# Kernel optimization log

Hardware: AMD Instinct MI355X
Metric: run time of the kernel (lower is better)

## Reference

```python
import jax, jax.numpy as jnp
import numpy as np

NUM_ITER = 3
NUM_SLOTS = 8
SLOT_SIZE = 128
MLP_HIDDEN = 256
EPSILON = 1e-8
INPUT_SIZE = 128
LN_EPS = 1e-5


def layer_norm(x):
    # parameter-free LayerNorm over last dim (LayerNorm() built with no args)
    mu = jnp.mean(x, axis=-1, keepdims=True)
    var = jnp.mean(jnp.square(x - mu), axis=-1, keepdims=True)
    return (x - mu) * jax.lax.rsqrt(var + LN_EPS)


def setup_inputs() -> dict:
    key = jax.random.key(0)
    ks = jax.random.split(key, 16)
    B, N, Din, D, H = 128, 4096, INPUT_SIZE, SLOT_SIZE, MLP_HIDDEN
    s_in = 1.0 / np.sqrt(Din)
    s_d = 1.0 / np.sqrt(D)
    s_h = 1.0 / np.sqrt(H)
    return {
        "inputs": jax.random.normal(ks[0], (B, N, Din), jnp.float32),
        "slots_noise": jax.random.normal(ks[1], (B, NUM_SLOTS, D), jnp.float32),
        "slots_mu": jax.random.normal(ks[2], (1, 1, D), jnp.float32),
        "slots_log_sigma": jax.random.normal(ks[3], (1, 1, D), jnp.float32) * 0.1,
        "Wq": jax.random.normal(ks[4], (D, D), jnp.float32) * s_d,
        "Wk": jax.random.normal(ks[5], (D, Din), jnp.float32) * s_in,
        "Wv": jax.random.normal(ks[6], (D, Din), jnp.float32) * s_in,
        "W_ih": jax.random.normal(ks[7], (3 * D, D), jnp.float32) * s_d,
        "W_hh": jax.random.normal(ks[8], (3 * D, D), jnp.float32) * s_d,
        "b_ih": jax.random.normal(ks[9], (3 * D,), jnp.float32) * s_d,
        "b_hh": jax.random.normal(ks[10], (3 * D,), jnp.float32) * s_d,
        "W1": jax.random.normal(ks[11], (H, D), jnp.float32) * s_d,
        "b1": jnp.zeros((H,), jnp.float32),
        "W2": jax.random.normal(ks[12], (D, H), jnp.float32) * s_h,
        "b2": jnp.zeros((D,), jnp.float32),
    }


def gru_cell(x, h, W_ih, W_hh, b_ih, b_hh):
    # PyTorch GRU, single step. x, h: (..., D)
    gx = x @ W_ih.T + b_ih  # (..., 3D)
    gh = h @ W_hh.T + b_hh
    D = h.shape[-1]
    xr, xz, xn = gx[..., :D], gx[..., D:2 * D], gx[..., 2 * D:]
    hr, hz, hn = gh[..., :D], gh[..., D:2 * D], gh[..., 2 * D:]
    r = jax.nn.sigmoid(xr + hr)
    z = jax.nn.sigmoid(xz + hz)
    n = jnp.tanh(xn + r * hn)
    return (1.0 - z) * n + z * h


def reference(inputs, slots_noise, slots_mu, slots_log_sigma, Wq, Wk, Wv,
              W_ih, W_hh, b_ih, b_hh, W1, b1, W2, b2):
    scale = 1.0 / np.sqrt(SLOT_SIZE)
    x = layer_norm(inputs)                      # (B, N, Din)
    k = x @ Wk.T                                # (B, N, D)
    v = x @ Wv.T                                # (B, N, D)
    slots = slots_mu + jnp.exp(slots_log_sigma) * slots_noise  # (B, S, D)
    for _ in range(NUM_ITER):
        slots_n = layer_norm(slots)             # NOTE: GRU hidden is the NORMED slots (matches source)
        q = slots_n @ Wq.T                      # (B, S, D)
        logits = jnp.einsum("bnd,bsd->bns", k, q) * scale  # (B, N, S)
        attn = jax.nn.softmax(logits, axis=-1) + EPSILON
        attn = attn / jnp.sum(attn, axis=-2, keepdims=True)
        updates = jnp.einsum("bns,bnd->bsd", attn, v)      # (B, S, D)
        slots = gru_cell(updates, slots_n, W_ih, W_hh, b_ih, b_hh)
        slots = slots + (jax.nn.relu(layer_norm(slots) @ W1.T + b1) @ W2.T + b2)
    return slots
```

## Files before the change

kernel.cpp:

```cpp
#include <hip/hip_runtime.h>
#include <math.h>


typedef __attribute__((ext_vector_type(4))) float fx4;
typedef __attribute__((ext_vector_type(8))) short sx8;
typedef __attribute__((ext_vector_type(4))) short sx4;
typedef __attribute__((ext_vector_type(8))) __bf16 bfx8;
typedef __attribute__((ext_vector_type(4))) unsigned short ux4;

static __device__ __forceinline__ fx4 MFMA(sx8 a, sx8 b, fx4 c) {
  return __builtin_amdgcn_mfma_f32_16x16x32_bf16(
      __builtin_bit_cast(bfx8, a), __builtin_bit_cast(bfx8, b), c, 0, 0, 0);
}

static __device__ __forceinline__ unsigned short f2bf(float f) {
  union { float f; unsigned u; } x; x.f = f;
  unsigned r = x.u + 0x7fffu + ((x.u >> 16) & 1u);
  return (unsigned short)(r >> 16);
}
static __device__ __forceinline__ float bf2f(unsigned short u) {
  union { unsigned u; float f; } x; x.u = ((unsigned)u) << 16; return x.f;
}
static __device__ __forceinline__ fx4 ntload4(const float* p) {
  return __builtin_nontemporal_load((const fx4*)p);
}

#define PSTR 72

__global__ __launch_bounds__(256) void k_fold(
    const float* __restrict__ Wq, const float* __restrict__ Wk,
    const float* __restrict__ Wih, const float* __restrict__ Wv,
    float* __restrict__ Wqk, float* __restrict__ Wihv) {
  int idx = blockIdx.x * 256 + threadIdx.x;
  if (idx < 16384) {
    int e = idx >> 7, c = idx & 127;
    float s = 0.f;
#pragma unroll 4
    for (int d = 0; d < 128; d++) s += Wq[d * 128 + e] * Wk[d * 128 + c];
    Wqk[idx] = s * 0.08838834764831845f;
    return;
  }
  idx -= 16384;
// ... 1 lines not shown
    int g = idx >> 7, c = idx & 127;
    float s = 0.f;
#pragma unroll 4
    for (int d = 0; d < 128; d++) s += Wih[g * 128 + d] * Wv[d * 128 + c];
    Wihv[idx] = s;
  }
}

__global__ __launch_bounds__(256) void k_pack(
    const float* __restrict__ noise, const float* __restrict__ mu,
    const float* __restrict__ lsig, const float* __restrict__ Wqk,
    const float* __restrict__ Wihv, const float* __restrict__ Whh,
    const float* __restrict__ W1, const float* __restrict__ W2,
    float* __restrict__ slots, unsigned short* __restrict__ wqk_b,
    unsigned short* __restrict__ wihv_b, unsigned short* __restrict__ whh_b,
    unsigned short* __restrict__ w1_b, unsigned short* __restrict__ w2_b) {
  int idx = blockIdx.x * 256 + threadIdx.x;
  if (idx < 131072) {
    int d = idx & 127;
    slots[idx] = mu[d] + expf(lsig[d]) * noise[idx];
    return;
  }
  idx -= 131072;
  if (idx < 16384) {
    wqk_b[idx] = f2bf(Wqk[(idx & 127) * 128 + (idx >> 7)]);
    return;
  }
  idx -= 16384;
  if (idx < 49152) { wihv_b[idx] = f2bf(Wihv[idx]); return; }
  idx -= 49152;
  if (idx < 49152) { whh_b[idx] = f2bf(Whh[idx]); return; }
  idx -= 49152;
  if (idx < 32768) { w1_b[idx] = f2bf(W1[idx]); return; }
  idx -= 32768;
  w2_b[idx] = f2bf(W2[idx]);
}

__global__ __launch_bounds__(64) void k_slot_pre(
    const float* __restrict__ slots, const unsigned short* __restrict__ wqk_b,
    float* __restrict__ slots_n, unsigned short* __restrict__ q2_b) {
  __shared__ __align__(16) short xf[4 * 64 * 8];
  int l = threadIdx.x;
  int r = l & 15, seg = l >> 4;
  long rowbase = (long)blockIdx.x * 16;
  {
    const float* xp = slots + (rowbase + r) * 128 + seg * 32;
    float* snp = slots_n + (rowbase + r) * 128 + seg * 32;
    float v[32];
    float s = 0.f, s2 = 0.f;
#pragma unroll
// ... 33 lines not shown
    sx8 a = *(const sx8*)&xf[(ks * 64 + l) * 8];
#pragma unroll
    for (int nt = 0; nt < 8; nt++) {
      sx8 bfr = *(const sx8*)(wqk_b + (nt * 16 + (l & 15)) * 128 + ks * 32 + (l >> 4) * 8);
      acc[nt] = MFMA(a, bfr, acc[nt]);
    }
  }
  int cl = l & 15, rq = (l >> 4) * 4;
#pragma unroll
  for (int nt = 0; nt < 8; nt++)
#pragma unroll
    for (int rg = 0; rg < 4; rg++)
      q2_b[(rowbase + rq + rg) * 128 + nt * 16 + cl] = f2bf(acc[nt][rg]);
}

__global__ __launch_bounds__(256, 4) void k_attn(
    const unsigned short* __restrict__ ln16, const unsigned short* __restrict__ q2b,
    float* __restrict__ upd_part, float* __restrict__ sattn_part) {
  __shared__ __align__(16) float abuf[4 * 1024];
  __shared__ __align__(16) short plds[4][2][16 * PSTR];
  __shared__ float sattnbuf[4 * 8];
  int tid = threadIdx.x, w = tid >> 6, l = tid & 63;
  int b = blockIdx.x >> 4, c = blockIdx.x & 15;
  long base = (long)b * 4096 + (c * 4 + w) * 64;
  const unsigned short* xt = ln16 + base * 128;
  int nr = l & 15, seg = l >> 4, qd = seg * 8;
  sx8 qf[4];
#pragma unroll
  for (int ks = 0; ks < 4; ks++) {
    if (nr < 8) {
      qf[ks] = *(const sx8*)(q2b + ((long)b * 8 + nr) * 128 + ks * 32 + qd);
    } else {
      sx8 t;
#pragma unroll
      for (int j = 0; j < 8; j++) t[j] = 0;
      qf[ks] = t;
    }
  }
  const fx4 z4 = {0.f, 0.f, 0.f, 0.f};
  float satacc[4] = {0.f, 0.f, 0.f, 0.f};
  short* ph = &plds[w][0][0];
  short* pl = &plds[w][1][0];
#pragma unroll
  for (int mt = 0; mt < 4; mt++) {
    fx4 cc = z4;
#pragma unroll
    for (int ks = 0; ks < 4; ks++) {
      sx8 bfr = *(const sx8*)(xt + (mt * 16 + nr) * 128 + ks * 32 + qd);
      cc = MFMA(qf[ks], bfr, cc);
    }
    float m01 = fmaxf(fmaxf(cc[0], cc[1]), fmaxf(cc[2], cc[3]));
    m01 = fmaxf(m01, __shfl_xor(m01, 16, 64));
    float p0 = __expf(cc[0] - m01), p1 = __expf(cc[1] - m01),
          p2 = __expf(cc[2] - m01), p3 = __expf(cc[3] - m01);
    float sl = p0 + p1 + p2 + p3;
    sl += __shfl_xor(sl, 16, 64);
    float inv = 1.f / sl;
    float at0 = p0 * inv + 1e-8f, at1 = p1 * inv + 1e-8f;
    float at2 = p2 * inv + 1e-8f, at3 = p3 * inv + 1e-8f;
    satacc[0] += at0; satacc[1] += at1; satacc[2] += at2; satacc[3] += at3;
    int pbase = mt * 16 + nr;
    unsigned short h0 = f2bf(at0), h1 = f2bf(at1), h2 = f2bf(at2), h3 = f2bf(at3);
    ph[(seg * 4 + 0) * PSTR + pbase] = (short)h0;
    ph[(seg * 4 + 1) * PSTR + pbase] = (short)h1;
    ph[(seg * 4 + 2) * PSTR + pbase] = (short)h2;
    ph[(seg * 4 + 3) * PSTR + pbase] = (short)h3;
    pl[(seg * 4 + 0) * PSTR + pbase] = (short)f2bf(at0 - bf2f(h0));
    pl[(seg * 4 + 1) * PSTR + pbase] = (short)f2bf(at1 - bf2f(h1));
    pl[(seg * 4 + 2) * PSTR + pbase] = (short)f2bf(at2 - bf2f(h2));
    pl[(seg * 4 + 3) * PSTR + pbase] = (short)f2bf(at3 - bf2f(h3));
  }
  fx4 acc[8];
#pragma unroll
  for (int nt = 0; nt < 8; nt++) acc[nt] = z4;
#pragma unroll
  for (int ks2 = 0; ks2 < 2; ks2++) {
    sx8 pah = *(const sx8*)&ph[nr * PSTR + ks2 * 32 + seg * 8];
    sx8 pal = *(const sx8*)&pl[nr * PSTR + ks2 * 32 + seg * 8];
#pragma unroll
    for (int nt = 0; nt < 8; nt++) {
      const unsigned short* cp = xt + (ks2 * 32 + seg * 8) * 128 + nt * 16 + nr;
      sx8 bfr;
#pragma unroll
      for (int j = 0; j < 8; j++) bfr[j] = (short)cp[j * 128];
      acc[nt] = MFMA(pah, bfr, acc[nt]);
// ... 14 lines not shown
    v += __shfl_xor(v, 2, 64);
    v += __shfl_xor(v, 4, 64);
    v += __shfl_xor(v, 8, 64);
    if (nr == 0 && seg < 2) sattnbuf[w * 8 + seg * 4 + rg] = v;
  }
  __syncthreads();
  {
    int i = tid * 4;
    fx4 o = *(const fx4*)&abuf[i] + *(const fx4*)&abuf[1024 + i] +
            *(const fx4*)&abuf[2048 + i] + *(const fx4*)&abuf[3072 + i];
    *(fx4*)(upd_part + ((size_t)(b * 16 + c)) * 1024 + i) = o;
    if (tid < 8)
      sattn_part[(b * 16 + c) * 8 + tid] =
          sattnbuf[tid] + sattnbuf[8 + tid] + sattnbuf[16 + tid] + sattnbuf[24 + tid];
  }
}

__global__ __launch_bounds__(256, 4) void k_attn_first(
    const float* __restrict__ x, unsigned short* __restrict__ ln16,
    const unsigned short* __restrict__ q2b,
    float* __restrict__ upd_part, float* __restrict__ sattn_part) {
  __shared__ __align__(16) float abuf[4 * 1024];
  __shared__ __align__(16) short plds[4][2][16 * PSTR];
  __shared__ float sattnbuf[4 * 8];
  int tid = threadIdx.x, w = tid >> 6, l = tid & 63;
  int b = blockIdx.x >> 4, c = blockIdx.x & 15;
  long base = (long)b * 4096 + (c * 4 + w) * 64;
  const float* xs = x + base * 128;
  unsigned short* xt = ln16 + base * 128;
  int nr = l & 15, seg = l >> 4, qd = seg * 8;
  sx8 qf[4];
#pragma unroll
  for (int ks = 0; ks < 4; ks++) {
    if (nr < 8) {
      qf[ks] = *(const sx8*)(q2b + ((long)b * 8 + nr) * 128 + ks * 32 + qd);
    } else {
      sx8 t;
#pragma unroll
      for (int j = 0; j < 8; j++) t[j] = 0;
      qf[ks] = t;
    }
  }
  const fx4 z4 = {0.f, 0.f, 0.f, 0.f};
  float satacc[4] = {0.f, 0.f, 0.f, 0.f};
  short* ph = &plds[w][0][0];
  short* pl = &plds[w][1][0];
#pragma unroll
  for (int mt = 0; mt < 4; mt++) {
    const float* rp = xs + (mt * 16 + nr) * 128 + qd;
    float v[32];
    float sm = 0.f, s2 = 0.f;
#pragma unroll
    for (int ks = 0; ks < 4; ks++) {
      fx4 t0 = ntload4(rp + ks * 32);
      fx4 t1 = ntload4(rp + ks * 32 + 4);
      v[ks * 8 + 0] = t0.x; v[ks * 8 + 1] = t0.y; v[ks * 8 + 2] = t0.z; v[ks * 8 + 3] = t0.w;
      v[ks * 8 + 4] = t1.x; v[ks * 8 + 5] = t1.y; v[ks * 8 + 6] = t1.z; v[ks * 8 + 7] = t1.w;
      sm += t0.x + t0.y + t0.z + t0.w + t1.x + t1.y + t1.z + t1.w;
      s2 += t0.x * t0.x + t0.y * t0.y + t0.z * t0.z + t0.w * t0.w +
            t1.x * t1.x + t1.y * t1.y + t1.z * t1.z + t1.w * t1.w;
    }
// ... 8 lines not shown
#pragma unroll
      for (int j = 0; j < 8; j++) t[j] = (short)f2bf((v[ks * 8 + j] - mean) * rstd);
      *(sx8*)(xt + (mt * 16 + nr) * 128 + ks * 32 + qd) = t;
      cc = MFMA(qf[ks], t, cc);
    }
    float m01 = fmaxf(fmaxf(cc[0], cc[1]), fmaxf(cc[2], cc[3]));
    m01 = fmaxf(m01, __shfl_xor(m01, 16, 64));
    float p0 = __expf(cc[0] - m01), p1 = __expf(cc[1] - m01),
          p2 = __expf(cc[2] - m01), p3 = __expf(cc[3] - m01);
    float sl = p0 + p1 + p2 + p3;
    sl += __shfl_xor(sl, 16, 64);
    float inv = 1.f / sl;
    float at0 = p0 * inv + 1e-8f, at1 = p1 * inv + 1e-8f;
    float at2 = p2 * inv + 1e-8f, at3 = p3 * inv + 1e-8f;
    satacc[0] += at0; satacc[1] += at1; satacc[2] += at2; satacc[3] += at3;
    int pbase = mt * 16 + nr;
    unsigned short h0 = f2bf(at0), h1 = f2bf(at1), h2 = f2bf(at2), h3 = f2bf(at3);
    ph[(seg * 4 + 0) * PSTR + pbase] = (short)h0;
    ph[(seg * 4 + 1) * PSTR + pbase] = (short)h1;
    ph[(seg * 4 + 2) * PSTR + pbase] = (short)h2;
    ph[(seg * 4 + 3) * PSTR + pbase] = (short)h3;
    pl[(seg * 4 + 0) * PSTR + pbase] = (short)f2bf(at0 - bf2f(h0));
    pl[(seg * 4 + 1) * PSTR + pbase] = (short)f2bf(at1 - bf2f(h1));
    pl[(seg * 4 + 2) * PSTR + pbase] = (short)f2bf(at2 - bf2f(h2));
    pl[(seg * 4 + 3) * PSTR + pbase] = (short)f2bf(at3 - bf2f(h3));
  }
  __threadfence_block();
  fx4 acc[8];
#pragma unroll
  for (int nt = 0; nt < 8; nt++) acc[nt] = z4;
#pragma unroll
  for (int ks2 = 0; ks2 < 2; ks2++) {
    sx8 pah = *(const sx8*)&ph[nr * PSTR + ks2 * 32 + seg * 8];
    sx8 pal = *(const sx8*)&pl[nr * PSTR + ks2 * 32 + seg * 8];
#pragma unroll
    for (int nt = 0; nt < 8; nt++) {
      const unsigned short* cp = xt + (ks2 * 32 + seg * 8) * 128 + nt * 16 + nr;
      sx8 bfr;
#pragma unroll
      for (int j = 0; j < 8; j++) bfr[j] = (short)cp[j * 128];
// ... 15 lines not shown
    v += __shfl_xor(v, 2, 64);
    v += __shfl_xor(v, 4, 64);
    v += __shfl_xor(v, 8, 64);
    if (nr == 0 && seg < 2) sattnbuf[w * 8 + seg * 4 + rg] = v;
  }
  __syncthreads();
  {
    int i = tid * 4;
    fx4 o = *(const fx4*)&abuf[i] + *(const fx4*)&abuf[1024 + i] +
            *(const fx4*)&abuf[2048 + i] + *(const fx4*)&abuf[3072 + i];
    *(fx4*)(upd_part + ((size_t)(b * 16 + c)) * 1024 + i) = o;
    if (tid < 8)
      sattn_part[(b * 16 + c) * 8 + tid] =
          sattnbuf[tid] + sattnbuf[8 + tid] + sattnbuf[16 + tid] + sattnbuf[24 + tid];
  }
}

__global__ __launch_bounds__(256) void k_slot_post(
    const float* __restrict__ upd_part, const float* __restrict__ sattn_part,
    float* __restrict__ slots_n,
    const unsigned short* __restrict__ wihv_b, const unsigned short* __restrict__ whh_b,
    const float* __restrict__ b_ih, const float* __restrict__ b_hh,
    const unsigned short* __restrict__ w1_b, const float* __restrict__ b1,
    const unsigned short* __restrict__ w2_b, const float* __restrict__ b2,
    const unsigned short* __restrict__ wqk_b,
    unsigned short* __restrict__ q2_b, float* __restrict__ out_final, int final_flag) {
  __shared__ __align__(16) char smem[78336];
  float* gx = (float*)smem;
  float* gh = (float*)(smem + 24576);
  float* xred = gx;
  short* xfr = (short*)(smem + 49152);
  short* hfr = (short*)(smem + 53248);
  short* ynf = (short*)(smem + 57344);
  short* y1f = (short*)(smem + 61440);
  float* snew = (float*)(smem + 69632);
  float* satred = (float*)(smem + 78080);
  int tid = threadIdx.x, w = tid >> 6, l = tid & 63;
  int rowbase = blockIdx.x * 16;
  int r = l & 15, seg = l >> 4;
  {
    int row = rowbase + r;
    int bb = row >> 3, ss = row & 7;
    float a[32];
#pragma unroll
    for (int i = 0; i < 32; i++) a[i] = 0.f;
    float satsum = 0.f;
#pragma unroll
    for (int ci = 0; ci < 4; ci++) {
      int ch = bb * 16 + w * 4 + ci;
      const float* up = upd_part + (size_t)ch * 1024 + ss * 128 + seg * 32;
#pragma unroll
      for (int i = 0; i < 8; i++) {
        fx4 t = *(const fx4*)(up + i * 4);
        a[i * 4 + 0] += t.x; a[i * 4 + 1] += t.y; a[i * 4 + 2] += t.z; a[i * 4 + 3] += t.w;
      }
      satsum += sattn_part[ch * 8 + ss];
    }
#pragma unroll
    for (int i = 0; i < 8; i++) {
      fx4 t = {a[i * 4], a[i * 4 + 1], a[i * 4 + 2], a[i * 4 + 3]};
      *(fx4*)&xred[w * 2048 + r * 128 + seg * 32 + i * 4] = t;
    }
    if (seg == 0) satred[w * 16 + r] = satsum;
  }
  __syncthreads();
  if (w == 0) {
    float inv = 1.f / (satred[r] + satred[16 + r] + satred[32 + r] + satred[48 + r]);
    float a[32];
#pragma unroll
    for (int i = 0; i < 8; i++) {
      fx4 t = *(const fx4*)&xred[r * 128 + seg * 32 + i * 4];
      fx4 t1 = *(const fx4*)&xred[2048 + r * 128 + seg * 32 + i * 4];
      fx4 t2 = *(const fx4*)&xred[4096 + r * 128 + seg * 32 + i * 4];
      fx4 t3 = *(const fx4*)&xred[6144 + r * 128 + seg * 32 + i * 4];
      t = t + t1 + t2 + t3;
      a[i * 4 + 0] = t.x * inv; a[i * 4 + 1] = t.y * inv;
      a[i * 4 + 2] = t.z * inv; a[i * 4 + 3] = t.w * inv;
    }
#pragma unroll
    for (int q = 0; q < 4; q++) {
      sx8 t;
#pragma unroll
      for (int j = 0; j < 8; j++) t[j] = (short)f2bf(a[q * 8 + j]);
      *(sx8*)&xfr[(seg * 64 + (r + 16 * q)) * 8] = t;
    }
  } else if (w == 1) {
    const float* hp = slots_n + (long)(rowbase + r) * 128 + seg * 32;
#pragma unroll
    for (int q = 0; q < 4; q++) {
      fx4 t0 = *(const fx4*)(hp + q * 8);
      fx4 t1 = *(const fx4*)(hp + q * 8 + 4);
      sx8 t;
      t[0] = (short)f2bf(t0.x); t[1] = (short)f2bf(t0.y);
      t[2] = (short)f2bf(t0.z); t[3] = (short)f2bf(t0.w);
      t[4] = (short)f2bf(t1.x); t[5] = (short)f2bf(t1.y);
      t[6] = (short)f2bf(t1.z); t[7] = (short)f2bf(t1.w);
      *(sx8*)&hfr[(seg * 64 + (r + 16 * q)) * 8] = t;
    }
  }
  __syncthreads();
  const fx4 z4 = {0.f, 0.f, 0.f, 0.f};
  {
    fx4 ax[6], ah[6];
#pragma unroll
    for (int j = 0; j < 6; j++) { ax[j] = z4; ah[j] = z4; }
#pragma unroll
    for (int ks = 0; ks < 4; ks++) {
      sx8 a_x = *(const sx8*)&xfr[(ks * 64 + l) * 8];
      sx8 a_h = *(const sx8*)&hfr[(ks * 64 + l) * 8];
#pragma unroll
      for (int j = 0; j < 6; j++) {
        int nt = w * 6 + j;
        sx8 bx = *(const sx8*)(wihv_b + (nt * 16 + (l & 15)) * 128 + ks * 32 + (l >> 4) * 8);
        sx8 bh = *(const sx8*)(whh_b + (nt * 16 + (l & 15)) * 128 + ks * 32 + (l >> 4) * 8);
        ax[j] = MFMA(a_x, bx, ax[j]);
        ah[j] = MFMA(a_h, bh, ah[j]);
      }
    }
#pragma unroll
    for (int j = 0; j < 6; j++) {
      int col = (w * 6 + j) * 16 + (l & 15);
#pragma unroll
      for (int rg = 0; rg < 4; rg++) {
        int row = (l >> 4) * 4 + rg;
        gx[row * 384 + col] = ax[j][rg];
        gh[row * 384 + col] = ah[j][rg];
      }
    }
  }
  __syncthreads();
  {
    int row = tid >> 4, j0 = (tid & 15) * 8;
#pragma unroll
    for (int j = j0; j < j0 + 8; j++) {
      float xr = gx[row * 384 + j] + b_ih[j];
      float xz = gx[row * 384 + 128 + j] + b_ih[128 + j];
      float xn = gx[row * 384 + 256 + j] + b_ih[256 + j];
      float hr = gh[row * 384 + j] + b_hh[j];
      float hz = gh[row * 384 + 128 + j] + b_hh[128 + j];
      float hn = gh[row * 384 + 256 + j] + b_hh[256 + j];
      float rr = 1.f / (1.f + __expf(-(xr + hr)));
      float zz = 1.f / (1.f + __expf(-(xz + hz)));
      float nn = tanhf(xn + rr * hn);
      float h = slots_n[(long)(rowbase + row) * 128 + j];
      snew[row * 132 + j] = (1.f - zz) * nn + zz * h;
    }
  }
  __syncthreads();
  if (w == 0) {
    float v[32];
    float s = 0.f, s2 = 0.f;
#pragma unroll
    for (int i = 0; i < 32; i++) {
      float t = snew[r * 132 + seg * 32 + i];
      v[i] = t; s += t; s2 += t * t;
    }
    s += __shfl_xor(s, 16, 64);  s += __shfl_xor(s, 32, 64);
    s2 += __shfl_xor(s2, 16, 64); s2 += __shfl_xor(s2, 32, 64);
    float mean = s * 0.0078125f;
    float var = s2 * 0.0078125f - mean * mean;
    float rstd = rsqrtf(var + 1e-5f);
#pragma unroll
    for (int q = 0; q < 4; q++) {
      sx8 t;
#pragma unroll
      for (int j = 0; j < 8; j++) t[j] = (short)f2bf((v[q * 8 + j] - mean) * rstd);
      *(sx8*)&ynf[(seg * 64 + (r + 16 * q)) * 8] = t;
    }
  }
  __syncthreads();
  {
    fx4 y[4];
#pragma unroll
    for (int j = 0; j < 4; j++) y[j] = z4;
#pragma unroll
    for (int ks = 0; ks < 4; ks++) {
      sx8 a = *(const sx8*)&ynf[(ks * 64 + l) * 8];
#pragma unroll
      for (int j = 0; j < 4; j++) {
        int nt = w * 4 + j;
        sx8 bf = *(const sx8*)(w1_b + (nt * 16 + (l & 15)) * 128 + ks * 32 + (l >> 4) * 8);
        y[j] = MFMA(a, bf, y[j]);
      }
    }
#pragma unroll
    for (int j = 0; j < 4; j++) {
      int col = (w * 4 + j) * 16 + (l & 15);
      float bias = b1[col];
      int ks3 = col >> 5, qq = (col >> 3) & 3, jj = col & 7;
#pragma unroll
      for (int rg = 0; rg < 4; rg++) {
        float val = fmaxf(y[j][rg] + bias, 0.f);
        int m = (l >> 4) * 4 + rg;
        y1f[(ks3 * 64 + m + 16 * qq) * 8 + jj] = (short)f2bf(val);
      }
    }
  }
  __syncthreads();
  {
    fx4 zz2[2];
    zz2[0] = z4; zz2[1] = z4;
#pragma unroll
    for (int ks = 0; ks < 8; ks++) {
      sx8 a = *(const sx8*)&y1f[(ks * 64 + l) * 8];
#pragma unroll
      for (int j = 0; j < 2; j++) {
        sx8 bf = *(const sx8*)(w2_b + ((w * 2 + j) * 16 + (l & 15)) * 256 + ks * 32 + (l >> 4) * 8);
        zz2[j] = MFMA(a, bf, zz2[j]);
      }
    }
#pragma unroll
    for (int j = 0; j < 2; j++) {
      int col = (w * 2 + j) * 16 + (l & 15);
      float bias = b2[col];
#pragma unroll
      for (int rg = 0; rg < 4; rg++) {
        int row = (l >> 4) * 4 + rg;
        snew[row * 132 + col] += zz2[j][rg] + bias;
      }
    }
  }
  __syncthreads();
  if (final_flag) {
    int row = tid >> 4, c8 = (tid & 15) * 8;
    fx4 t0 = *(const fx4*)&snew[row * 132 + c8];
    fx4 t1 = *(const fx4*)&snew[row * 132 + c8 + 4];
    *(fx4*)(out_final + (long)(rowbase + row) * 128 + c8) = t0;
    *(fx4*)(out_final + (long)(rowbase + row) * 128 + c8 + 4) = t1;
    return;
  }
  if (w == 0) {
    float v[32];
    float s = 0.f, s2 = 0.f;
#pragma unroll
    for (int i = 0; i < 32; i++) {
      float t = snew[r * 132 + seg * 32 + i];
      v[i] = t; s += t; s2 += t * t;
    }
    s += __shfl_xor(s, 16, 64);  s += __shfl_xor(s, 32, 64);
    s2 += __shfl_xor(s2, 16, 64); s2 += __shfl_xor(s2, 32, 64);
    float mean = s * 0.0078125f;
    float var = s2 * 0.0078125f - mean * mean;
    float rstd = rsqrtf(var + 1e-5f);
    float* snp = slots_n + (long)(rowbase + r) * 128 + seg * 32;
#pragma unroll
    for (int i = 0; i < 8; i++) {
      fx4 t = {(v[i * 4 + 0] - mean) * rstd, (v[i * 4 + 1] - mean) * rstd,
               (v[i * 4 + 2] - mean) * rstd, (v[i * 4 + 3] - mean) * rstd};
      *(fx4*)(snp + i * 4) = t;
      v[i * 4 + 0] = t.x; v[i * 4 + 1] = t.y; v[i * 4 + 2] = t.z; v[i * 4 + 3] = t.w;
    }
#pragma unroll
    for (int q = 0; q < 4; q++) {
      sx8 t;
#pragma unroll
      for (int j = 0; j < 8; j++) t[j] = (short)f2bf(v[q * 8 + j]);
      *(sx8*)&ynf[(seg * 64 + (r + 16 * q)) * 8] = t;
    }
  }
  __syncthreads();
  {
    fx4 acc2[2];
    acc2[0] = z4; acc2[1] = z4;
#pragma unroll
    for (int ks = 0; ks < 4; ks++) {
      sx8 a = *(const sx8*)&ynf[(ks * 64 + l) * 8];
#pragma unroll
      for (int j = 0; j < 2; j++) {
        int nt = w * 2 + j;
        sx8 bf = *(const sx8*)(wqk_b + (nt * 16 + (l & 15)) * 128 + ks * 32 + (l >> 4) * 8);
        acc2[j] = MFMA(a, bf, acc2[j]);
      }
    }
    int cl = l & 15, rq = (l >> 4) * 4;
#pragma unroll
    for (int j = 0; j < 2; j++) {
      int nt = w * 2 + j;
#pragma unroll
      for (int rg = 0; rg < 4; rg++)
        q2_b[(long)(rowbase + rq + rg) * 128 + nt * 16 + cl] = f2bf(acc2[j][rg]);
    }
  }
}

extern "C" void kernel_launch(void* const* d_in, const int* in_sizes, int n_in,
                              void* d_out, int out_size, void* d_ws, size_t ws_size,
                              hipStream_t stream) {
  (void)in_sizes; (void)n_in; (void)out_size; (void)ws_size;
  const float* x = (const float*)d_in[0];
  const float* noise = (const float*)d_in[1];
  const float* mu = (const float*)d_in[2];
  const float* lsig = (const float*)d_in[3];
  const float* Wq = (const float*)d_in[4];
  const float* Wk = (const float*)d_in[5];
  const float* Wv = (const float*)d_in[6];
  const float* Wih = (const float*)d_in[7];
  const float* Whh = (const float*)d_in[8];
// ... 12 lines not shown
    return p;
  };
  unsigned short* ln16 = (unsigned short*)take(134217728);
  float* Wqk = (float*)take(65536);
  float* Wihv = (float*)take(196608);
  unsigned short* wqk_b = (unsigned short*)take(32768);
  unsigned short* wihv_b = (unsigned short*)take(98304);
  unsigned short* whh_b = (unsigned short*)take(98304);
  unsigned short* w1_b = (unsigned short*)take(65536);
  unsigned short* w2_b = (unsigned short*)take(65536);
  float* slots = (float*)take(524288);
  float* slots_n = (float*)take(524288);
  unsigned short* q2_b = (unsigned short*)take(262144);
  float* upd_part = (float*)take(8388608);
  float* sattn_part = (float*)take(65536);

  k_fold<<<256, 256, 0, stream>>>(Wq, Wk, Wih, Wv, Wqk, Wihv);
  k_pack<<<1216, 256, 0, stream>>>(noise, mu, lsig, Wqk, Wihv, Whh, W1, W2,
                                   slots, wqk_b, wihv_b, whh_b, w1_b, w2_b);
  k_slot_pre<<<64, 64, 0, stream>>>(slots, wqk_b, slots_n, q2_b);
  k_attn_first<<<2048, 256, 0, stream>>>(x, ln16, q2_b, upd_part, sattn_part);
  k_slot_post<<<64, 256, 0, stream>>>(upd_part, sattn_part, slots_n, wihv_b, whh_b,
                                      b_ih, b_hh, w1_b, b1, w2_b, b2, wqk_b,
                                      q2_b, (float*)d_out, 0);
  for (int it = 1; it < 3; it++) {
    k_attn<<<2048, 256, 0, stream>>>(ln16, q2_b, upd_part, sattn_part);
    k_slot_post<<<64, 256, 0, stream>>>(upd_part, sattn_part, slots_n, wihv_b, whh_b,
                                        b_ih, b_hh, w1_b, b1, w2_b, b2, wqk_b,
                                        q2_b, (float*)d_out, (it == 2) ? 1 : 0);
  }
}
```

Measured before the change: 577.8 us.

## Fuse slot update into attention kernel via last-block atomic counter

Removes the separate k_slot_post launches by having the last finishing attention block of each group of two batches (32 blocks, 16 slot rows) run the GRU, MLP and next-query computation, signalled by an atomic counter that k_pack zeroes. It also reworks the GRU so each wave computes its r/z/n gate tiles in registers and applies the gates directly, dropping the large shared-memory staging of gx and gh. This cuts launch gaps and the tail of the small 64-block slot kernel, allowing slot updates to overlap with other attention blocks. The trade-offs are threadfence plus atomic overhead in every block, and the slot work running inside the attention kernel's shared-memory and occupancy limits.

```diff
diff --git a/kernel.cpp b/kernel.cpp
--- a/kernel.cpp
+++ b/kernel.cpp
@@ -26,6 +26,7 @@
 }
 
 #define PSTR 72
+#define SMEM_BYTES 34944
 
 __global__ __launch_bounds__(256) void k_fold(
     const float* __restrict__ Wq, const float* __restrict__ Wk,
@@ -57,7 +58,8 @@
     const float* __restrict__ W1, const float* __restrict__ W2,
     float* __restrict__ slots, unsigned short* __restrict__ wqk_b,
     unsigned short* __restrict__ wihv_b, unsigned short* __restrict__ whh_b,
-    unsigned short* __restrict__ w1_b, unsigned short* __restrict__ w2_b) {
+    unsigned short* __restrict__ w1_b, unsigned short* __restrict__ w2_b,
+    unsigned* __restrict__ cnt) {
   int idx = blockIdx.x * 256 + threadIdx.x;
   if (idx < 131072) {
     int d = idx & 127;
@@ -76,7 +78,9 @@
   idx -= 49152;
   if (idx < 32768) { w1_b[idx] = f2bf(W1[idx]); return; }
   idx -= 32768;
-  w2_b[idx] = f2bf(W2[idx]);
+  if (idx < 32768) { w2_b[idx] = f2bf(W2[idx]); return; }
+  idx -= 32768;
+  if (idx < 192) cnt[idx] = 0;
 }
 
 __global__ __launch_bounds__(64) void k_slot_pre(
@@ -140,12 +144,253 @@
       q2_b[(rowbase + rq + rg) * 128 + nt * 16 + cl] = f2bf(acc[nt][rg]);
 }
 
-__global__ __launch_bounds__(256, 4) void k_attn(
+static __device__ __forceinline__ void slot_post_body(
+    char* smem, int tid, int rowbase,
+    const float* __restrict__ upd_part, const float* __restrict__ sattn_part,
+    float* __restrict__ slots_n,
+    const unsigned short* __restrict__ wihv_b, const unsigned short* __restrict__ whh_b,
+    const float* __restrict__ b_ih, const float* __restrict__ b_hh,
+    const unsigned short* __restrict__ w1_b, const float* __restrict__ b1,
+    const unsigned short* __restrict__ w2_b, const float* __restrict__ b2,
+    const unsigned short* __restrict__ wqk_b, unsigned short* __restrict__ q2_b,
+    float* __restrict__ out_final, int final_flag) {
+  short* xfr = (short*)smem;
+  short* hfr = (short*)(smem + 4096);
+  short* ynf = (short*)(smem + 8192);
+  short* y1f = (short*)(smem + 12288);
+  float* snew = (float*)(smem + 20480);
+  float* satred = (float*)(smem + 28928);
+  int w = tid >> 6, l = tid & 63;
+  int r = l & 15, seg = l >> 4;
+  const fx4 z4 = {0.f, 0.f, 0.f, 0.f};
+  {
+    int tr = tid & 15, tc = tid >> 4;
+    int row = rowbase + tr;
+    int bb = row >> 3, ss = row & 7;
+    fx4 a0 = z4, a1 = z4;
+#pragma unroll 4
+    for (int ci = 0; ci < 16; ci++) {
+      const float* up = upd_part + (size_t)(bb * 16 + ci) * 1024 + ss * 128 + tc * 8;
+      a0 += *(const fx4*)up;
+      a1 += *(const fx4*)(up + 4);
+    }
+    if (tc == 0) {
+      float ssum = 0.f;
+#pragma unroll 4
+      for (int ci = 0; ci < 16; ci++) ssum += sattn_part[(bb * 16 + ci) * 8 + ss];
+      satred[tr] = ssum;
+    }
+    {
+      const float* hp = slots_n + (long)row * 128 + tc * 8;
+      fx4 t0 = *(const fx4*)hp, t1 = *(const fx4*)(hp + 4);
+      sx8 t;
+      t[0] = (short)f2bf(t0.x); t[1] = (short)f2bf(t0.y);
+      t[2] = (short)f2bf(t0.z); t[3] = (short)f2bf(t0.w);
+      t[4] = (short)f2bf(t1.x); t[5] = (short)f2bf(t1.y);
+      t[6] = (short)f2bf(t1.z); t[7] = (short)f2bf(t1.w);
+      int ks = tc >> 2, q = tc & 3;
+      *(sx8*)&hfr[(ks * 64 + tr + 16 * q) * 8] = t;
+    }
+    __syncthreads();
+    float inv = 1.f / satred[tr];
+    sx8 t;
+    t[0] = (short)f2bf(a0.x * inv); t[1] = (short)f2bf(a0.y * inv);
+    t[2] = (short)f2bf(a0.z * inv); t[3] = (short)f2bf(a0.w * inv);
+    t[4] = (short)f2bf(a1.x * inv); t[5] = (short)f2bf(a1.y * inv);
+    t[6] = (short)f2bf(a1.z * inv); t[7] = (short)f2bf(a1.w * inv);
+    int ks = tc >> 2, q = tc & 3;
+    *(sx8*)&xfr[(ks * 64 + tr + 16 * q) * 8] = t;
+  }
+  __syncthreads();
+  {
+    fx4 ax[6], ah[6];
+#pragma unroll
+    for (int j = 0; j < 6; j++) { ax[j] = z4; ah[j] = z4; }
+    int cl = l & 15;
+#pragma unroll
+    for (int ks = 0; ks < 4; ks++) {
+      sx8 a_x = *(const sx8*)&xfr[(ks * 64 + l) * 8];
+      sx8 a_h = *(const sx8*)&hfr[(ks * 64 + l) * 8];
+#pragma unroll
+      for (int j = 0; j < 6; j++) {
+        int nt = w * 2 + (j & 1) + (j >> 1) * 8;
+        sx8 bx = *(const sx8*)(wihv_b + (nt * 16 + cl) * 128 + ks * 32 + seg * 8);
+        sx8 bh = *(const sx8*)(whh_b + (nt * 16 + cl) * 128 + ks * 32 + seg * 8);
+        ax[j] = MFMA(a_x, bx, ax[j]);
+        ah[j] = MFMA(a_h, bh, ah[j]);
+      }
+    }
+#pragma unroll
+    for (int jj = 0; jj < 2; jj++) {
+      int col = (w * 2 + jj) * 16 + cl;
+      float bir = b_ih[col], biz = b_ih[128 + col], bin = b_ih[256 + col];
+      float bhr = b_hh[col], bhz = b_hh[128 + col], bhn = b_hh[256 + col];
+#pragma unroll
+      for (int rg = 0; rg < 4; rg++) {
+        int row = seg * 4 + rg;
+        float xr = ax[jj][rg] + bir, xz = ax[jj + 2][rg] + biz, xnn = ax[jj + 4][rg] + bin;
+        float hr = ah[jj][rg] + bhr, hz = ah[jj + 2][rg] + bhz, hnn = ah[jj + 4][rg] + bhn;
+        float rr = 1.f / (1.f + __expf(-(xr + hr)));
+        float zz = 1.f / (1.f + __expf(-(xz + hz)));
+        float nn = tanhf(xnn + rr * hnn);
+        float h = slots_n[(long)(rowbase + row) * 128 + col];
+        snew[row * 132 + col] = (1.f - zz) * nn + zz * h;
+      }
+    }
+  }
+  __syncthreads();
+  if (w == 0) {
+    float v[32];
+    float s = 0.f, s2 = 0.f;
+#pragma unroll
+    for (int i = 0; i < 32; i++) {
+      float t = snew[r * 132 + seg * 32 + i];
+      v[i] = t; s += t; s2 += t * t;
+    }
+    s += __shfl_xor(s, 16, 64);  s += __shfl_xor(s, 32, 64);
+    s2 += __shfl_xor(s2, 16, 64); s2 += __shfl_xor(s2, 32, 64);
+    float mean = s * 0.0078125f;
+    float var = s2 * 0.0078125f - mean * mean;
+    float rstd = rsqrtf(var + 1e-5f);
+#pragma unroll
+    for (int q = 0; q < 4; q++) {
+      sx8 t;
+#pragma unroll
+      for (int j = 0; j < 8; j++) t[j] = (short)f2bf((v[q * 8 + j] - mean) * rstd);
+      *(sx8*)&ynf[(seg * 64 + (r + 16 * q)) * 8] = t;
+    }
+  }
+  __syncthreads();
+  {
+    fx4 y[4];
+#pragma unroll
+    for (int j = 0; j < 4; j++) y[j] = z4;
+#pragma unroll
+    for (int ks = 0; ks < 4; ks++) {
+      sx8 a = *(const sx8*)&ynf[(ks * 64 + l) * 8];
+#pragma unroll
+      for (int j = 0; j < 4; j++) {
+        int nt = w * 4 + j;
+        sx8 bf = *(const sx8*)(w1_b + (nt * 16 + (l & 15)) * 128 + ks * 32 + (l >> 4) * 8);
+        y[j] = MFMA(a, bf, y[j]);
+      }
+    }
+#pragma unroll
+    for (int j = 0; j < 4; j++) {
+      int col = (w * 4 + j) * 16 + (l & 15);
+      float bias = b1[col];
+      int ks3 = col >> 5, qq = (col >> 3) & 3, jj = col & 7;
+#pragma unroll
+      for (int rg = 0; rg < 4; rg++) {
+        float val = fmaxf(y[j][rg] + bias, 0.f);
+        int m = (l >> 4) * 4 + rg;
+        y1f[(ks3 * 64 + m + 16 * qq) * 8 + jj] = (short)f2bf(val);
+      }
+    }
+  }
+  __syncthreads();
+  {
+    fx4 zz2[2];
+    zz2[0] = z4; zz2[1] = z4;
+#pragma unroll
+    for (int ks = 0; ks < 8; ks++) {
+      sx8 a = *(const sx8*)&y1f[(ks * 64 + l) * 8];
+#pragma unroll
+      for (int j = 0; j < 2; j++) {
+        sx8 bf = *(const sx8*)(w2_b + ((w * 2 + j) * 16 + (l & 15)) * 256 + ks * 32 + (l >> 4) * 8);
+        zz2[j] = MFMA(a, bf, zz2[j]);
+      }
+    }
+#pragma unroll
+    for (int j = 0; j < 2; j++) {
+      int col = (w * 2 + j) * 16 + (l & 15);
+      float bias = b2[col];
+#pragma unroll
+      for (int rg = 0; rg < 4; rg++) {
+        int row = (l >> 4) * 4 + rg;
+        snew[row * 132 + col] += zz2[j][rg] + bias;
+      }
+    }
+  }
+  __syncthreads();
+  if (final_flag) {
+    int row = tid >> 4, c8 = (tid & 15) * 8;
+    fx4 t0 = *(const fx4*)&snew[row * 132 + c8];
+    fx4 t1 = *(const fx4*)&snew[row * 132 + c8 + 4];
+    *(fx4*)(out_final + (long)(rowbase + row) * 128 + c8) = t0;
+    *(fx4*)(out_final + (long)(rowbase + row) * 128 + c8 + 4) = t1;
+    return;
+  }
+  if (w == 0) {
+    float v[32];
+    float s = 0.f, s2 = 0.f;
+#pragma unroll
+    for (int i = 0; i < 32; i++) {
+      float t = snew[r * 132 + seg * 32 + i];
+      v[i] = t; s += t; s2 += t * t;
+    }
+    s += __shfl_xor(s, 16, 64);  s += __shfl_xor(s, 32, 64);
+    s2 += __shfl_xor(s2, 16, 64); s2 += __shfl_xor(s2, 32, 64);
+    float mean = s * 0.0078125f;
+    float var = s2 * 0.0078125f - mean * mean;
+    float rstd = rsqrtf(var + 1e-5f);
+    float* snp = slots_n + (long)(rowbase + r) * 128 + seg * 32;
+#pragma unroll
+    for (int i = 0; i < 8; i++) {
+      fx4 t = {(v[i * 4 + 0] - mean) * rstd, (v[i * 4 + 1] - mean) * rstd,
+               (v[i * 4 + 2] - mean) * rstd, (v[i * 4 + 3] - mean) * rstd};
+      *(fx4*)(snp + i * 4) = t;
+      v[i * 4 + 0] = t.x; v[i * 4 + 1] = t.y; v[i * 4 + 2] = t.z; v[i * 4 + 3] = t.w;
+    }
+#pragma unroll
+    for (int q = 0; q < 4; q++) {
+      sx8 t;
+#pragma unroll
+      for (int j = 0; j < 8; j++) t[j] = (short)f2bf(v[q * 8 + j]);
+      *(sx8*)&ynf[(seg * 64 + (r + 16 * q)) * 8] = t;
+    }
+  }
+  __syncthreads();
+  {
+    fx4 acc2[2];
+    acc2[0] = z4; acc2[1] = z4;
+#pragma unroll
+    for (int ks = 0; ks < 4; ks++) {
+      sx8 a = *(const sx8*)&ynf[(ks * 64 + l) * 8];
+#pragma unroll
+      for (int j = 0; j < 2; j++) {
+        int nt = w * 2 + j;
+        sx8 bf = *(const sx8*)(wqk_b + (nt * 16 + (l & 15)) * 128 + ks * 32 + (l >> 4) * 8);
+        acc2[j] = MFMA(a, bf, acc2[j]);
+      }
+    }
+    int cl = l & 15, rq = (l >> 4) * 4;
+#pragma unroll
+    for (int j = 0; j < 2; j++) {
+      int nt = w * 2 + j;
+#pragma unroll
+      for (int rg = 0; rg < 4; rg++)
+        q2_b[(long)(rowbase + rq + rg) * 128 + nt * 16 + cl] = f2bf(acc2[j][rg]);
+    }
+  }
+}
+
+__global__ __launch_bounds__(256, 4) void k_iter(
     const unsigned short* __restrict__ ln16, const unsigned short* __restrict__ q2b,
-    float* __restrict__ upd_part, float* __restrict__ sattn_part) {
-  __shared__ __align__(16) float abuf[4 * 1024];
-  __shared__ __align__(16) short plds[4][2][16 * PSTR];
-  __shared__ float sattnbuf[4 * 8];
+    float* __restrict__ upd_part, float* __restrict__ sattn_part,
+    unsigned* __restrict__ pcnt,
+    float* __restrict__ slots_n,
+    const unsigned short* __restrict__ wihv_b, const unsigned short* __restrict__ whh_b,
+    const float* __restrict__ b_ih, const float* __restrict__ b_hh,
+    const unsigned short* __restrict__ w1_b, const float* __restrict__ b1,
+    const unsigned short* __restrict__ w2_b, const float* __restrict__ b2,
+    const unsigned short* __restrict__ wqk_b, unsigned short* __restrict__ q2_b,
+    float* __restrict__ out_final, int final_flag) {
+  __shared__ __align__(16) char smem[SMEM_BYTES];
+  __shared__ unsigned tail_done;
+  float* abuf = (float*)smem;
+  short* pbase = (short*)(smem + 16384);
+  float* sattnbuf = (float*)(smem + 16384 + 18432);
   int tid = threadIdx.x, w = tid >> 6, l = tid & 63;
   int b = blockIdx.x >> 4, c = blockIdx.x & 15;
   long base = (long)b * 4096 + (c * 4 + w) * 64;
@@ -165,8 +410,8 @@
   }
   const fx4 z4 = {0.f, 0.f, 0.f, 0.f};
   float satacc[4] = {0.f, 0.f, 0.f, 0.f};
-  short* ph = &plds[w][0][0];
-  short* pl = &plds[w][1][0];
+  short* ph = pbase + (w * 2) * (16 * PSTR);
+  short* pl = pbase + (w * 2 + 1) * (16 * PSTR);
 #pragma unroll
   for (int mt = 0; mt < 4; mt++) {
     fx4 cc = z4;
@@ -185,16 +430,16 @@
     float at0 = p0 * inv + 1e-8f, at1 = p1 * inv + 1e-8f;
     float at2 = p2 * inv + 1e-8f, at3 = p3 * inv + 1e-8f;
     satacc[0] += at0; satacc[1] += at1; satacc[2] += at2; satacc[3] += at3;
-    int pbase = mt * 16 + nr;
+    int pb = mt * 16 + nr;
     unsigned short h0 = f2bf(at0), h1 = f2bf(at1), h2 = f2bf(at2), h3 = f2bf(at3);
-    ph[(seg * 4 + 0) * PSTR + pbase] = (short)h0;
-    ph[(seg * 4 + 1) * PSTR + pbase] = (short)h1;
-    ph[(seg * 4 + 2) * PSTR + pbase] = (short)h2;
-    ph[(seg * 4 + 3) * PSTR + pbase] = (short)h3;
-    pl[(seg * 4 + 0) * PSTR + pbase] = (short)f2bf(at0 - bf2f(h0));
-    pl[(seg * 4 + 1) * PSTR + pbase] = (short)f2bf(at1 - bf2f(h1));
-    pl[(seg * 4 + 2) * PSTR + pbase] = (short)f2bf(at2 - bf2f(h2));
-    pl[(seg * 4 + 3) * PSTR + pbase] = (short)f2bf(at3 - bf2f(h3));
+    ph[(seg * 4 + 0) * PSTR + pb] = (short)h0;
+    ph[(seg * 4 + 1) * PSTR + pb] = (short)h1;
+    ph[(seg * 4 + 2) * PSTR + pb] = (short)h2;
+    ph[(seg * 4 + 3) * PSTR + pb] = (short)h3;
+    pl[(seg * 4 + 0) * PSTR + pb] = (short)f2bf(at0 - bf2f(h0));
+    pl[(seg * 4 + 1) * PSTR + pb] = (short)f2bf(at1 - bf2f(h1));
+    pl[(seg * 4 + 2) * PSTR + pb] = (short)f2bf(at2 - bf2f(h2));
+    pl[(seg * 4 + 3) * PSTR + pb] = (short)f2bf(at3 - bf2f(h3));
   }
   fx4 acc[8];
 #pragma unroll
@@ -239,15 +484,33 @@
       sattn_part[(b * 16 + c) * 8 + tid] =
           sattnbuf[tid] + sattnbuf[8 + tid] + sattnbuf[16 + tid] + sattnbuf[24 + tid];
   }
-}
-
-__global__ __launch_bounds__(256, 4) void k_attn_first(
+  __threadfence();
+  if (tid == 0) tail_done = (atomicAdd(&pcnt[b >> 1], 1u) == 31u) ? 1u : 0u;
+  __syncthreads();
+  if (!tail_done) return;
+  __threadfence();
+  slot_post_body(smem, tid, (b >> 1) * 16, upd_part, sattn_part, slots_n,
+                 wihv_b, whh_b, b_ih, b_hh, w1_b, b1, w2_b, b2, wqk_b, q2_b,
+                 out_final, final_flag);
+}
+
+__global__ __launch_bounds__(256, 4) void k_iter_first(
     const float* __restrict__ x, unsigned short* __restrict__ ln16,
     const unsigned short* __restrict__ q2b,
-    float* __restrict__ upd_part, float* __restrict__ sattn_part) {
-  __shared__ __align__(16) float abuf[4 * 1024];
-  __shared__ __align__(16) short plds[4][2][16 * PSTR];
-  __shared__ float sattnbuf[4 * 8];
+    float* __restrict__ upd_part, float* __restrict__ sattn_part,
+    unsigned* __restrict__ pcnt,
+    float* __restrict__ slots_n,
+    const unsigned short* __restrict__ wihv_b, const unsigned short* __restrict__ whh_b,
+    const float* __restrict__ b_ih, const float* __restrict__ b_hh,
+    const unsigned short* __restrict__ w1_b, const float* __restrict__ b1,
+    const unsigned short* __restrict__ w2_b, const float* __restrict__ b2,
+    const unsigned short* __restrict__ wqk_b, unsigned short* __restrict__ q2_b,
+    float* __restrict__ out_final, int final_flag) {
+  __shared__ __align__(16) char smem[SMEM_BYTES];
+  __shared__ unsigned tail_done;
+  float* abuf = (float*)smem;
+  short* pbase = (short*)(smem + 16384);
+  float* sattnbuf = (float*)(smem + 16384 + 18432);
   int tid = threadIdx.x, w = tid >> 6, l = tid & 63;
   int b = blockIdx.x >> 4, c = blockIdx.x & 15;
   long base = (long)b * 4096 + (c * 4 + w) * 64;
@@ -268,8 +531,8 @@
   }
   const fx4 z4 = {0.f, 0.f, 0.f, 0.f};
   float satacc[4] = {0.f, 0.f, 0.f, 0.f};
-  short* ph = &plds[w][0][0];
-  short* pl = &plds[w][1][0];
+  short* ph = pbase + (w * 2) * (16 * PSTR);
+  short* pl = pbase + (w * 2 + 1) * (16 * PSTR);
 #pragma unroll
   for (int mt = 0; mt < 4; mt++) {
     const float* rp = xs + (mt * 16 + nr) * 128 + qd;
@@ -308,16 +571,16 @@
     float at0 = p0 * inv + 1e-8f, at1 = p1 * inv + 1e-8f;
     float at2 = p2 * inv + 1e-8f, at3 = p3 * inv + 1e-8f;
     satacc[0] += at0; satacc[1] += at1; satacc[2] += at2; satacc[3] += at3;
-    int pbase = mt * 16 + nr;
+    int pb = mt * 16 + nr;
     unsigned short h0 = f2bf(at0), h1 = f2bf(at1), h2 = f2bf(at2), h3 = f2bf(at3);
-    ph[(seg * 4 + 0) * PSTR + pbase] = (short)h0;
-    ph[(seg * 4 + 1) * PSTR + pbase] = (short)h1;
-    ph[(seg * 4 + 2) * PSTR + pbase] = (short)h2;
-    ph[(seg * 4 + 3) * PSTR + pbase] = (short)h3;
-    pl[(seg * 4 + 0) * PSTR + pbase] = (short)f2bf(at0 - bf2f(h0));
-    pl[(seg * 4 + 1) * PSTR + pbase] = (short)f2bf(at1 - bf2f(h1));
-    pl[(seg * 4 + 2) * PSTR + pbase] = (short)f2bf(at2 - bf2f(h2));
-    pl[(seg * 4 + 3) * PSTR + pbase] = (short)f2bf(at3 - bf2f(h3));
+    ph[(seg * 4 + 0) * PSTR + pb] = (short)h0;
+    ph[(seg * 4 + 1) * PSTR + pb] = (short)h1;
+    ph[(seg * 4 + 2) * PSTR + pb] = (short)h2;
+    ph[(seg * 4 + 3) * PSTR + pb] = (short)h3;
+    pl[(seg * 4 + 0) * PSTR + pb] = (short)f2bf(at0 - bf2f(h0));
+    pl[(seg * 4 + 1) * PSTR + pb] = (short)f2bf(at1 - bf2f(h1));
+    pl[(seg * 4 + 2) * PSTR + pb] = (short)f2bf(at2 - bf2f(h2));
+    pl[(seg * 4 + 3) * PSTR + pb] = (short)f2bf(at3 - bf2f(h3));
   }
   __threadfence_block();
   fx4 acc[8];
@@ -363,273 +626,14 @@
       sattn_part[(b * 16 + c) * 8 + tid] =
           sattnbuf[tid] + sattnbuf[8 + tid] + sattnbuf[16 + tid] + sattnbuf[24 + tid];
   }
-}
-
-__global__ __launch_bounds__(256) void k_slot_post(
-    const float* __restrict__ upd_part, const float* __restrict__ sattn_part,
-    float* __restrict__ slots_n,
-    const unsigned short* __restrict__ wihv_b, const unsigned short* __restrict__ whh_b,
-    const float* __restrict__ b_ih, const float* __restrict__ b_hh,
-    const unsigned short* __restrict__ w1_b, const float* __restrict__ b1,
-    const unsigned short* __restrict__ w2_b, const float* __restrict__ b2,
-    const unsigned short* __restrict__ wqk_b,
-    unsigned short* __restrict__ q2_b, float* __restrict__ out_final, int final_flag) {
-  __shared__ __align__(16) char smem[78336];
-  float* gx = (float*)smem;
-  float* gh = (float*)(smem + 24576);
-  float* xred = gx;
-  short* xfr = (short*)(smem + 49152);
-  short* hfr = (short*)(smem + 53248);
-  short* ynf = (short*)(smem + 57344);
-  short* y1f = (short*)(smem + 61440);
-  float* snew = (float*)(smem + 69632);
-  float* satred = (float*)(smem + 78080);
-  int tid = threadIdx.x, w = tid >> 6, l = tid & 63;
-  int rowbase = blockIdx.x * 16;
-  int r = l & 15, seg = l >> 4;
-  {
-    int row = rowbase + r;
-    int bb = row >> 3, ss = row & 7;
-    float a[32];
-#pragma unroll
-    for (int i = 0; i < 32; i++) a[i] = 0.f;
-    float satsum = 0.f;
-#pragma unroll
-    for (int ci = 0; ci < 4; ci++) {
-      int ch = bb * 16 + w * 4 + ci;
-      const float* up = upd_part + (size_t)ch * 1024 + ss * 128 + seg * 32;
-#pragma unroll
-      for (int i = 0; i < 8; i++) {
-        fx4 t = *(const fx4*)(up + i * 4);
-        a[i * 4 + 0] += t.x; a[i * 4 + 1] += t.y; a[i * 4 + 2] += t.z; a[i * 4 + 3] += t.w;
-      }
-      satsum += sattn_part[ch * 8 + ss];
-    }
-#pragma unroll
-    for (int i = 0; i < 8; i++) {
-      fx4 t = {a[i * 4], a[i * 4 + 1], a[i * 4 + 2], a[i * 4 + 3]};
-      *(fx4*)&xred[w * 2048 + r * 128 + seg * 32 + i * 4] = t;
-    }
-    if (seg == 0) satred[w * 16 + r] = satsum;
-  }
-  __syncthreads();
-  if (w == 0) {
-    float inv = 1.f / (satred[r] + satred[16 + r] + satred[32 + r] + satred[48 + r]);
-    float a[32];
-#pragma unroll
-    for (int i = 0; i < 8; i++) {
-      fx4 t = *(const fx4*)&xred[r * 128 + seg * 32 + i * 4];
-      fx4 t1 = *(const fx4*)&xred[2048 + r * 128 + seg * 32 + i * 4];
-      fx4 t2 = *(const fx4*)&xred[4096 + r * 128 + seg * 32 + i * 4];
-      fx4 t3 = *(const fx4*)&xred[6144 + r * 128 + seg * 32 + i * 4];
-      t = t + t1 + t2 + t3;
-      a[i * 4 + 0] = t.x * inv; a[i * 4 + 1] = t.y * inv;
-      a[i * 4 + 2] = t.z * inv; a[i * 4 + 3] = t.w * inv;
-    }
-#pragma unroll
-    for (int q = 0; q < 4; q++) {
-      sx8 t;
-#pragma unroll
-      for (int j = 0; j < 8; j++) t[j] = (short)f2bf(a[q * 8 + j]);
-      *(sx8*)&xfr[(seg * 64 + (r + 16 * q)) * 8] = t;
-    }
-  } else if (w == 1) {
-    const float* hp = slots_n + (long)(rowbase + r) * 128 + seg * 32;
-#pragma unroll
-    for (int q = 0; q < 4; q++) {
-      fx4 t0 = *(const fx4*)(hp + q * 8);
-      fx4 t1 = *(const fx4*)(hp + q * 8 + 4);
-      sx8 t;
-      t[0] = (short)f2bf(t0.x); t[1] = (short)f2bf(t0.y);
-      t[2] = (short)f2bf(t0.z); t[3] = (short)f2bf(t0.w);
-      t[4] = (short)f2bf(t1.x); t[5] = (short)f2bf(t1.y);
-      t[6] = (short)f2bf(t1.z); t[7] = (short)f2bf(t1.w);
-      *(sx8*)&hfr[(seg * 64 + (r + 16 * q)) * 8] = t;
-    }
-  }
-  __syncthreads();
-  const fx4 z4 = {0.f, 0.f, 0.f, 0.f};
-  {
-    fx4 ax[6], ah[6];
-#pragma unroll
-    for (int j = 0; j < 6; j++) { ax[j] = z4; ah[j] = z4; }
-#pragma unroll
-    for (int ks = 0; ks < 4; ks++) {
-      sx8 a_x = *(const sx8*)&xfr[(ks * 64 + l) * 8];
-      sx8 a_h = *(const sx8*)&hfr[(ks * 64 + l) * 8];
-#pragma unroll
-      for (int j = 0; j < 6; j++) {
-        int nt = w * 6 + j;
-        sx8 bx = *(const sx8*)(wihv_b + (nt * 16 + (l & 15)) * 128 + ks * 32 + (l >> 4) * 8);
-        sx8 bh = *(const sx8*)(whh_b + (nt * 16 + (l & 15)) * 128 + ks * 32 + (l >> 4) * 8);
-        ax[j] = MFMA(a_x, bx, ax[j]);
-        ah[j] = MFMA(a_h, bh, ah[j]);
-      }
-    }
-#pragma unroll
-    for (int j = 0; j < 6; j++) {
-      int col = (w * 6 + j) * 16 + (l & 15);
-#pragma unroll
-      for (int rg = 0; rg < 4; rg++) {
-        int row = (l >> 4) * 4 + rg;
-        gx[row * 384 + col] = ax[j][rg];
-        gh[row * 384 + col] = ah[j][rg];
-      }
-    }
-  }
-  __syncthreads();
-  {
-    int row = tid >> 4, j0 = (tid & 15) * 8;
-#pragma unroll
-    for (int j = j0; j < j0 + 8; j++) {
-      float xr = gx[row * 384 + j] + b_ih[j];
-      float xz = gx[row * 384 + 128 + j] + b_ih[128 + j];
-      float xn = gx[row * 384 + 256 + j] + b_ih[256 + j];
-      float hr = gh[row * 384 + j] + b_hh[j];
-      float hz = gh[row * 384 + 128 + j] + b_hh[128 + j];
-      float hn = gh[row * 384 + 256 + j] + b_hh[256 + j];
-      float rr = 1.f / (1.f + __expf(-(xr + hr)));
-      float zz = 1.f / (1.f + __expf(-(xz + hz)));
-      float nn = tanhf(xn + rr * hn);
-      float h = slots_n[(long)(rowbase + row) * 128 + j];
-      snew[row * 132 + j] = (1.f - zz) * nn + zz * h;
-    }
-  }
-  __syncthreads();
-  if (w == 0) {
-    float v[32];
-    float s = 0.f, s2 = 0.f;
-#pragma unroll
-    for (int i = 0; i < 32; i++) {
-      float t = snew[r * 132 + seg * 32 + i];
-      v[i] = t; s += t; s2 += t * t;
-    }
-    s += __shfl_xor(s, 16, 64);  s += __shfl_xor(s, 32, 64);
-    s2 += __shfl_xor(s2, 16, 64); s2 += __shfl_xor(s2, 32, 64);
-    float mean = s * 0.0078125f;
-    float var = s2 * 0.0078125f - mean * mean;
-    float rstd = rsqrtf(var + 1e-5f);
-#pragma unroll
-    for (int q = 0; q < 4; q++) {
-      sx8 t;
-#pragma unroll
-      for (int j = 0; j < 8; j++) t[j] = (short)f2bf((v[q * 8 + j] - mean) * rstd);
-      *(sx8*)&ynf[(seg * 64 + (r + 16 * q)) * 8] = t;
-    }
-  }
-  __syncthreads();
-  {
-    fx4 y[4];
-#pragma unroll
-    for (int j = 0; j < 4; j++) y[j] = z4;
-#pragma unroll
-    for (int ks = 0; ks < 4; ks++) {
-      sx8 a = *(const sx8*)&ynf[(ks * 64 + l) * 8];
-#pragma unroll
-      for (int j = 0; j < 4; j++) {
-        int nt = w * 4 + j;
-        sx8 bf = *(const sx8*)(w1_b + (nt * 16 + (l & 15)) * 128 + ks * 32 + (l >> 4) * 8);
-        y[j] = MFMA(a, bf, y[j]);
-      }
-    }
-#pragma unroll
-    for (int j = 0; j < 4; j++) {
-      int col = (w * 4 + j) * 16 + (l & 15);
-      float bias = b1[col];
-      int ks3 = col >> 5, qq = (col >> 3) & 3, jj = col & 7;
-#pragma unroll
-      for (int rg = 0; rg < 4; rg++) {
-        float val = fmaxf(y[j][rg] + bias, 0.f);
-        int m = (l >> 4) * 4 + rg;
-        y1f[(ks3 * 64 + m + 16 * qq) * 8 + jj] = (short)f2bf(val);
-      }
-    }
-  }
-  __syncthreads();
-  {
-    fx4 zz2[2];
-    zz2[0] = z4; zz2[1] = z4;
-#pragma unroll
-    for (int ks = 0; ks < 8; ks++) {
-      sx8 a = *(const sx8*)&y1f[(ks * 64 + l) * 8];
-#pragma unroll
-      for (int j = 0; j < 2; j++) {
-        sx8 bf = *(const sx8*)(w2_b + ((w * 2 + j) * 16 + (l & 15)) * 256 + ks * 32 + (l >> 4) * 8);
-        zz2[j] = MFMA(a, bf, zz2[j]);
-      }
-    }
-#pragma unroll
-    for (int j = 0; j < 2; j++) {
-      int col = (w * 2 + j) * 16 + (l & 15);
-      float bias = b2[col];
-#pragma unroll
-      for (int rg = 0; rg < 4; rg++) {
-        int row = (l >> 4) * 4 + rg;
-        snew[row * 132 + col] += zz2[j][rg] + bias;
-      }
-    }
-  }
-  __syncthreads();
-  if (final_flag) {
-    int row = tid >> 4, c8 = (tid & 15) * 8;
-    fx4 t0 = *(const fx4*)&snew[row * 132 + c8];
-    fx4 t1 = *(const fx4*)&snew[row * 132 + c8 + 4];
-    *(fx4*)(out_final + (long)(rowbase + row) * 128 + c8) = t0;
-    *(fx4*)(out_final + (long)(rowbase + row) * 128 + c8 + 4) = t1;
-    return;
-  }
-  if (w == 0) {
-    float v[32];
-    float s = 0.f, s2 = 0.f;
-#pragma unroll
-    for (int i = 0; i < 32; i++) {
-      float t = snew[r * 132 + seg * 32 + i];
-      v[i] = t; s += t; s2 += t * t;
-    }
-    s += __shfl_xor(s, 16, 64);  s += __shfl_xor(s, 32, 64);
-    s2 += __shfl_xor(s2, 16, 64); s2 += __shfl_xor(s2, 32, 64);
-    float mean = s * 0.0078125f;
-    float var = s2 * 0.0078125f - mean * mean;
-    float rstd = rsqrtf(var + 1e-5f);
-    float* snp = slots_n + (long)(rowbase + r) * 128 + seg * 32;
-#pragma unroll
-    for (int i = 0; i < 8; i++) {
-      fx4 t = {(v[i * 4 + 0] - mean) * rstd, (v[i * 4 + 1] - mean) * rstd,
-               (v[i * 4 + 2] - mean) * rstd, (v[i * 4 + 3] - mean) * rstd};
-      *(fx4*)(snp + i * 4) = t;
-      v[i * 4 + 0] = t.x; v[i * 4 + 1] = t.y; v[i * 4 + 2] = t.z; v[i * 4 + 3] = t.w;
-    }
-#pragma unroll
-    for (int q = 0; q < 4; q++) {
-      sx8 t;
-#pragma unroll
-      for (int j = 0; j < 8; j++) t[j] = (short)f2bf(v[q * 8 + j]);
-      *(sx8*)&ynf[(seg * 64 + (r + 16 * q)) * 8] = t;
-    }
-  }
-  __syncthreads();
-  {
-    fx4 acc2[2];
-    acc2[0] = z4; acc2[1] = z4;
-#pragma unroll
-    for (int ks = 0; ks < 4; ks++) {
-      sx8 a = *(const sx8*)&ynf[(ks * 64 + l) * 8];
-#pragma unroll
-      for (int j = 0; j < 2; j++) {
-        int nt = w * 2 + j;
-        sx8 bf = *(const sx8*)(wqk_b + (nt * 16 + (l & 15)) * 128 + ks * 32 + (l >> 4) * 8);
-        acc2[j] = MFMA(a, bf, acc2[j]);
-      }
-    }
-    int cl = l & 15, rq = (l >> 4) * 4;
-#pragma unroll
-    for (int j = 0; j < 2; j++) {
-      int nt = w * 2 + j;
-#pragma unroll
-      for (int rg = 0; rg < 4; rg++)
-        q2_b[(long)(rowbase + rq + rg) * 128 + nt * 16 + cl] = f2bf(acc2[j][rg]);
-    }
-  }
+  __threadfence();
+  if (tid == 0) tail_done = (atomicAdd(&pcnt[b >> 1], 1u) == 31u) ? 1u : 0u;
+  __syncthreads();
+  if (!tail_done) return;
+  __threadfence();
+  slot_post_body(smem, tid, (b >> 1) * 16, upd_part, sattn_part, slots_n,
+                 wihv_b, whh_b, b_ih, b_hh, w1_b, b1, w2_b, b2, wqk_b, q2_b,
+                 out_final, final_flag);
 }
 
 extern "C" void kernel_launch(void* const* d_in, const int* in_sizes, int n_in,
@@ -672,19 +676,22 @@
   unsigned short* q2_b = (unsigned short*)take(262144);
   float* upd_part = (float*)take(8388608);
   float* sattn_part = (float*)take(65536);
+  unsigned* cnt = (unsigned*)take(1024);
 
   k_fold<<<256, 256, 0, stream>>>(Wq, Wk, Wih, Wv, Wqk, Wihv);
-  k_pack<<<1216, 256, 0, stream>>>(noise, mu, lsig, Wqk, Wihv, Whh, W1, W2,
-                                   slots, wqk_b, wihv_b, whh_b, w1_b, w2_b);
+  k_pack<<<1217, 256, 0, stream>>>(noise, mu, lsig, Wqk, Wihv, Whh, W1, W2,
+                                   slots, wqk_b, wihv_b, whh_b, w1_b, w2_b, cnt);
   k_slot_pre<<<64, 64, 0, stream>>>(slots, wqk_b, slots_n, q2_b);
-  k_attn_first<<<2048, 256, 0, stream>>>(x, ln16, q2_b, upd_part, sattn_part);
-  k_slot_post<<<64, 256, 0, stream>>>(upd_part, sattn_part, slots_n, wihv_b, whh_b,
-                                      b_ih, b_hh, w1_b, b1, w2_b, b2, wqk_b,
-                                      q2_b, (float*)d_out, 0);
-  for (int it = 1; it < 3; it++) {
-    k_attn<<<2048, 256, 0, stream>>>(ln16, q2_b, upd_part, sattn_part);
-    k_slot_post<<<64, 256, 0, stream>>>(upd_part, sattn_part, slots_n, wihv_b, whh_b,
-                                        b_ih, b_hh, w1_b, b1, w2_b, b2, wqk_b,
-                                        q2_b, (float*)d_out, (it == 2) ? 1 : 0);
-  }
-}
+  k_iter_first<<<2048, 256, 0, stream>>>(x, ln16, q2_b, upd_part, sattn_part,
+                                         cnt, slots_n, wihv_b, whh_b, b_ih, b_hh,
+                                         w1_b, b1, w2_b, b2, wqk_b, q2_b,
+                                         (float*)d_out, 0);
+  k_iter<<<2048, 256, 0, stream>>>(ln16, q2_b, upd_part, sattn_part,
+                                   cnt + 64, slots_n, wihv_b, whh_b, b_ih, b_hh,
+                                   w1_b, b1, w2_b, b2, wqk_b, q2_b,
+                                   (float*)d_out, 0);
+  k_iter<<<2048, 256, 0, stream>>>(ln16, q2_b, upd_part, sattn_part,
+                                   cnt + 128, slots_n, wihv_b, whh_b, b_ih, b_hh,
+                                   w1_b, b1, w2_b, b2, wqk_b, q2_b,
+                                   (float*)d_out, 1);
+}
```

Result: slower. 1.730 ms (+199.5%).
